# Performance work log

Measured on AMD Instinct MI355X. Metric: run time of the kernel, lower is better.

The kernel has to match this reference:

```python
import jax, jax.numpy as jnp
import numpy as np

# Model config (matches init_kwargs)
L_F, DELTA_F, L_S, DELTA_S = 1, 1, 32, 16
HIDDEN = 32       # SSM state dim H
GRU_H = 64        # slow-branch GRU hidden
N_GRU = 4
B, T = 4, 32768


def setup_inputs() -> dict:
    key = jax.random.key(0)
    ks = jax.random.split(key, 13)
    def nrm(k, shape, s=0.05):
        return jax.random.normal(k, shape, dtype=jnp.float32) * s
    return {
        "x": jax.random.normal(ks[0], (B, T), dtype=jnp.float32),
        # SlowBranch params
        "fc_in_w": nrm(ks[1], (GRU_H, 1), 0.3),
        "fc_in_b": nrm(ks[2], (GRU_H,)),
        "gru_wih": nrm(ks[3], (N_GRU, 3 * GRU_H, GRU_H), 0.1),
        "gru_whh": nrm(ks[4], (N_GRU, 3 * GRU_H, GRU_H), 0.1),
        "gru_bih": nrm(ks[5], (N_GRU, 3 * GRU_H)),
        "gru_bhh": nrm(ks[6], (N_GRU, 3 * GRU_H)),
        "out_fc_w": nrm(ks[7], (2 * HIDDEN, GRU_H), 0.1),
        "out_fc_b": nrm(ks[8], (2 * HIDDEN,)),
        # Fast branch params (F_IN: 1->H, F_OUT: H->1)
        "fin_w": nrm(ks[9], (HIDDEN, 1), 0.3),
        "fin_b": nrm(ks[10], (HIDDEN,)),
        "fout_w": nrm(ks[11], (1, HIDDEN), 0.1),
        "fout_b": nrm(ks[12], (1,)),
    }


def _gru_layer(xs, Wih, Whh, bih, bhh):
    """Torch-convention GRU layer. xs: (N, L, H_in) -> (N, L, H)."""
    H = Whh.shape[1]
    # Precompute input-side gate pre-activations: (N, L, 3H)
    xp = jnp.einsum('nlh,gh->nlg', xs, Wih) + bih
    def step(h, xt):
        gh = h @ Whh.T + bhh                       # (N, 3H)
        ir, iz, inew = jnp.split(xt, 3, axis=-1)
        hr, hz, hnew = jnp.split(gh, 3, axis=-1)
        r = jax.nn.sigmoid(ir + hr)
        z = jax.nn.sigmoid(iz + hz)
        n = jnp.tanh(inew + r * hnew)
        h = (1.0 - z) * n + z * h
        return h, h
    h0 = jnp.zeros((xs.shape[0], H), xs.dtype)
    _, ys = jax.lax.scan(step, h0, jnp.swapaxes(xp, 0, 1))  # (L, N, H)
    return jnp.swapaxes(ys, 0, 1)


def reference(x, fc_in_w, fc_in_b, gru_wih, gru_whh, gru_bih, gru_bhh,
              out_fc_w, out_fc_b, fin_w, fin_b, fout_w, fout_b):
    Bsz, Tlen = x.shape
    num_slow = (Tlen - L_S) // DELTA_S + 1

    frame_idx = jnp.arange(num_slow)[:, None] * DELTA_S + jnp.arange(L_S)[None, :]
    x_s = x[:, frame_idx].reshape(Bsz * num_slow, L_S, 1)      # (N, L_s, 1)
    h = jax.nn.relu(x_s * fc_in_w[:, 0] + fc_in_b)             # (N, L_s, GRU_H)
    for l in range(gru_wih.shape[0]):
        h = _gru_layer(h, gru_wih[l], gru_whh[l], gru_bih[l], gru_bhh[l])
    eps = h[:, -1, :] @ out_fc_w.T + out_fc_b                  # (N, 2H)
    eps = eps.reshape(Bsz, num_slow, 2 * HIDDEN)
    A_slow = jax.nn.sigmoid(eps[..., :HIDDEN])                 # (B, S, H)
    g_slow = eps[..., HIDDEN:]                                 # (B, S, H)

    # ---- Fast branch: per-sample diagonal linear SSM scan ----
    delta = DELTA_S // DELTA_F
    idx = jnp.clip(jnp.arange(Tlen) // delta - 1, 0, num_slow - 1)  # (T,)
    A_t = A_slow[:, idx, :]                                    # (B, T, H)
    u_t = (x[..., None] * fin_w[:, 0] + fin_b) * g_slow[:, idx, :]  # (B, T, H)

    def step(hc, inp):
        A, u = inp
        hn = A * hc + u
        return hn, hn
    h0 = jnp.zeros((Bsz, HIDDEN), x.dtype)
    _, h_all = jax.lax.scan(step, h0,
                            (jnp.swapaxes(A_t, 0, 1), jnp.swapaxes(u_t, 0, 1)))
    # h_all: (T, B, H); F_OUT applied to every state
    return jnp.einsum('tbh,h->bt', h_all, fout_w[0]) + fout_b[0]   # (B, T)
```

## Files before the change

kernel.cpp:

```cpp
#include <hip/hip_runtime.h>
#include <hip/hip_bf16.h>

typedef __bf16 bf16x8 __attribute__((ext_vector_type(8)));
typedef short short8 __attribute__((ext_vector_type(8)));
typedef float f32x4 __attribute__((ext_vector_type(4)));
typedef unsigned short ushort_t;

#define T_LEN 32768
#define B_SZ 4
#define NSLOW 2047
#define NSEQ (B_SZ * NSLOW)
#define GH 64
#define G3 192
#define NL 4
#define HID 32
#define NCH 256
#define L2E 1.44269504088896341f

#define OFF_X    0
#define OFF_FCW  131072
#define OFF_FCB  131136
#define OFF_WIH  131200
#define OFF_WHH  180352
#define OFF_BIH  229504
#define OFF_BHH  230272
#define OFF_OFW  231040
#define OFF_OFB  235136
#define OFF_FINW 235200
#define OFF_FINB 235232
#define OFF_FOW  235264
#define OFF_FOB  235296
#define CONV_TOTAL 235297
#define CONV_PAD_BYTES 470656

static __device__ __forceinline__ float bf2f(ushort_t u) {
    union { unsigned u; float f; } c; c.u = ((unsigned)u) << 16; return c.f;
}
static __device__ __forceinline__ ushort_t f2bf(float f) {
    union { float f; unsigned u; } c; c.f = f;
    unsigned r = (c.u + 0x7FFFu + ((c.u >> 16) & 1u)) >> 16;
    return (ushort_t)r;
}
static __device__ __forceinline__ unsigned pk2bf(float a, float b) {
    float2 f; f.x = a; f.y = b;
    __hip_bfloat162 h = __float22bfloat162_rn(f);
    unsigned u;
    __builtin_memcpy(&u, &h, 4);
    return u;
}
static __device__ __forceinline__ f32x4 mfma16(short8 a, short8 b, f32x4 c) {
    return __builtin_amdgcn_mfma_f32_16x16x32_bf16(
        __builtin_bit_cast(bf16x8, a), __builtin_bit_cast(bf16x8, b), c, 0, 0, 0);
}
static __device__ __forceinline__ int xoff(int t, int kb, int seq) {
    return ((((t << 3) + kb) << 4) + (seq ^ (kb & 7))) << 3;
}
static __device__ __forceinline__ short8 load_frag_scaled(const ushort_t* p, float s) {
    uint4 r = *(const uint4*)p;
    unsigned aa[4] = {r.x, r.y, r.z, r.w};
    short8 o;
#pragma unroll
    for (int i = 0; i < 4; ++i) {
        o[2 * i]     = (short)f2bf(bf2f((ushort_t)(aa[i] & 0xffffu)) * s);
        o[2 * i + 1] = (short)f2bf(bf2f((ushort_t)(aa[i] >> 16)) * s);
    }
    return o;
}

struct Ptrs13 { const void* p[13]; };

__global__ __launch_bounds__(256) void convert_kernel(Ptrs13 ptrs,
                                                      int* __restrict__ flag,
                                                      ushort_t* __restrict__ dst)
{
    __shared__ int scnt;
    if (threadIdx.x == 0) scnt = 0;
    __syncthreads();
    {
        ushort_t u = ((const ushort_t*)ptrs.p[0])[threadIdx.x];
        int e = (u >> 7) & 0xFF;
        int ok = (e >= 80 && e <= 141) ? 1 : 0;
#pragma unroll
        for (int d = 1; d < 64; d <<= 1) ok += __shfl_xor(ok, d, 64);
        if ((threadIdx.x & 63) == 0) atomicAdd(&scnt, ok);
    }
    __syncthreads();
    const bool isbf = (scnt >= 224);
    if (blockIdx.x == 0 && threadIdx.x == 0) *flag = isbf ? 1 : 0;

    const int offs[14] = {OFF_X, OFF_FCW, OFF_FCB, OFF_WIH, OFF_WHH, OFF_BIH,
                          OFF_BHH, OFF_OFW, OFF_OFB, OFF_FINW, OFF_FINB,
                          OFF_FOW, OFF_FOB, CONV_TOTAL};
    for (int idx = blockIdx.x * 256 + threadIdx.x; idx < CONV_TOTAL;
         idx += gridDim.x * 256) {
        int s = 0;
#pragma unroll
        for (int j = 1; j < 13; ++j) if (idx >= offs[j]) s = j;
        int k = idx - offs[s];
        ushort_t v = isbf ? ((const ushort_t*)ptrs.p[s])[k]
                          : f2bf(((const float*)ptrs.p[s])[k]);
        dst[idx] = v;
    }
}

__global__ __launch_bounds__(256, 2) void gru_kernel(
    const ushort_t* __restrict__ x, const ushort_t* __restrict__ fcw,
    const ushort_t* __restrict__ fcb, const ushort_t* __restrict__ wih,
    const ushort_t* __restrict__ whh, const ushort_t* __restrict__ bih,
    const ushort_t* __restrict__ bhh, const ushort_t* __restrict__ ofw,
    const ushort_t* __restrict__ ofb, float* __restrict__ Aslow,
    float* __restrict__ gslow)
{
    __shared__ short8 Xs8[4096];
    short* Xs = (short*)Xs8;
    const int tid = threadIdx.x;
    const int w = tid >> 6, lane = tid & 63;
    const int q = lane >> 4, m = lane & 15;
    const int jb = w * 16;
    const int n0 = blockIdx.x * 16;

#pragma unroll 1
    for (int ii = 0; ii < 16; ++ii) {
        int cid = ii * 256 + tid;
        int seq = cid & 15, kb = (cid >> 4) & 7, t = cid >> 7;
        int n = n0 + seq; if (n > NSEQ - 1) n = NSEQ - 1;
        int b = n / NSLOW, s = n - b * NSLOW;
        float xv = bf2f(x[b * T_LEN + s * 16 + t]);
        short8 v;
#pragma unroll
        for (int i = 0; i < 8; ++i) {
            int g = kb * 8 + i;
            float h = fmaf(xv, bf2f(fcw[g]), bf2f(fcb[g]));
            h = h > 0.f ? h : 0.f;
            v[i] = (short)f2bf(h);
        }
        Xs8[xoff(t, kb, seq) >> 3] = v;
    }

    const int col0 = jb + 4 * q;
    const int kbw = (col0 >> 3);
    const int wsub = (col0 & 7);
    const int kofs = q * 8;
    const int wbase0 = ((kbw << 4) + (m ^ (kbw & 7))) * 8 + wsub;

    float hc[4];
#pragma unroll 1
    for (int l = 0; l < NL; ++l) {
        const ushort_t* wl = wih + l * G3 * GH;
        const ushort_t* ul = whh + l * G3 * GH;
        short8 wR0 = load_frag_scaled(wl + (0 * 64 + jb + m) * 64 + kofs, -L2E);
        short8 wR1 = load_frag_scaled(wl + (0 * 64 + jb + m) * 64 + 32 + kofs, -L2E);
        short8 wZ0 = load_frag_scaled(wl + (1 * 64 + jb + m) * 64 + kofs, -L2E);
        short8 wZ1 = load_frag_scaled(wl + (1 * 64 + jb + m) * 64 + 32 + kofs, -L2E);
        short8 wN0 = load_frag_scaled(wl + (2 * 64 + jb + m) * 64 + kofs, 2.f * L2E);
        short8 wN1 = load_frag_scaled(wl + (2 * 64 + jb + m) * 64 + 32 + kofs, 2.f * L2E);
        short8 uR0 = load_frag_scaled(ul + (0 * 64 + jb + m) * 64 + kofs, -L2E);
        short8 uR1 = load_frag_scaled(ul + (0 * 64 + jb + m) * 64 + 32 + kofs, -L2E);
        short8 uZ0 = load_frag_scaled(ul + (1 * 64 + jb + m) * 64 + kofs, -L2E);
        short8 uZ1 = load_frag_scaled(ul + (1 * 64 + jb + m) * 64 + 32 + kofs, -L2E);
        short8 uN0 = load_frag_scaled(ul + (2 * 64 + jb + m) * 64 + kofs, 2.f * L2E);
        short8 uN1 = load_frag_scaled(ul + (2 * 64 + jb + m) * 64 + 32 + kofs, 2.f * L2E);

        f32x4 bRv, bZv, bNXv, bNHv;
#pragma unroll
        for (int i = 0; i < 4; ++i) {
            int c = col0 + i;
            bRv[i]  = -L2E * (bf2f(bih[l * G3 + c]) + bf2f(bhh[l * G3 + c]));
            bZv[i]  = -L2E * (bf2f(bih[l * G3 + 64 + c]) + bf2f(bhh[l * G3 + 64 + c]));
            bNXv[i] = 2.f * L2E * bf2f(bih[l * G3 + 128 + c]);
            bNHv[i] = 2.f * L2E * bf2f(bhh[l * G3 + 128 + c]);
        }

        hc[0] = hc[1] = hc[2] = hc[3] = 0.f;

        __syncthreads();
        int iA = xoff(0, q, m) >> 3;
        int iB = xoff(0, 4 + q, m) >> 3;
        int wb = wbase0;

        short8 cx0 = Xs8[iA], cx1 = Xs8[iB];
        short8 nx0 = Xs8[iA + 128], nx1 = Xs8[iB + 128];
        f32x4 xR = bRv, xZ = bZv, xN = bNXv;
        xR = mfma16(wR0, cx0, xR); xR = mfma16(wR1, cx1, xR);
        xZ = mfma16(wZ0, cx0, xZ); xZ = mfma16(wZ1, cx1, xZ);
        xN = mfma16(wN0, cx0, xN); xN = mfma16(wN1, cx1, xN);
#pragma unroll
        for (int i = 0; i < 4; ++i) {
            float r = __builtin_amdgcn_rcpf(1.f + __builtin_amdgcn_exp2f(xR[i]));
            float z = __builtin_amdgcn_rcpf(1.f + __builtin_amdgcn_exp2f(xZ[i]));
            float yp = fmaf(r, bNHv[i], xN[i]);
            float nn = fmaf(-2.f,
                __builtin_amdgcn_rcpf(1.f + __builtin_amdgcn_exp2f(yp)), 1.f);
            hc[i] = fmaf(z, hc[i] - nn, nn);
        }
        *(uint2*)(Xs + wb) = make_uint2(pk2bf(hc[0], hc[1]), pk2bf(hc[2], hc[3]));
        xR = bRv; xZ = bZv; xN = bNXv;
        xR = mfma16(wR0, nx0, xR); xR = mfma16(wR1, nx1, xR);
        xZ = mfma16(wZ0, nx0, xZ); xZ = mfma16(wZ1, nx1, xZ);
        xN = mfma16(wN0, nx0, xN); xN = mfma16(wN1, nx1, xN);
        iA += 128; iB += 128; wb += 1024;

#pragma unroll 1
        for (int t = 1; t < 32; ++t) {
            __syncthreads();
            short8 bh0 = Xs8[iA - 128];
            short8 bh1 = Xs8[iB - 128];
            short8 px0, px1;
            if (t < 31) {
                px0 = Xs8[iA + 128];
                px1 = Xs8[iB + 128];
            }
            f32x4 aR = xR, aZ = xZ, aNH = bNHv;
            aR  = mfma16(uR0, bh0, aR);  aR  = mfma16(uR1, bh1, aR);
            aZ  = mfma16(uZ0, bh0, aZ);  aZ  = mfma16(uZ1, bh1, aZ);
            aNH = mfma16(uN0, bh0, aNH); aNH = mfma16(uN1, bh1, aNH);
#pragma unroll
            for (int i = 0; i < 4; ++i) {
                float r = __builtin_amdgcn_rcpf(1.f + __builtin_amdgcn_exp2f(aR[i]));
                float z = __builtin_amdgcn_rcpf(1.f + __builtin_amdgcn_exp2f(aZ[i]));
                float yp = fmaf(r, aNH[i], xN[i]);
                float nn = fmaf(-2.f,
                    __builtin_amdgcn_rcpf(1.f + __builtin_amdgcn_exp2f(yp)), 1.f);
                hc[i] = fmaf(z, hc[i] - nn, nn);
            }
            *(uint2*)(Xs + wb) =
                make_uint2(pk2bf(hc[0], hc[1]), pk2bf(hc[2], hc[3]));
            if (t < 31) {
                xR = bRv; xZ = bZv; xN = bNXv;
                xR = mfma16(wR0, px0, xR); xR = mfma16(wR1, px1, xR);
                xZ = mfma16(wZ0, px0, xZ); xZ = mfma16(wZ1, px1, xZ);
                xN = mfma16(wN0, px0, xN); xN = mfma16(wN1, px1, xN);
            }
            iA += 128; iB += 128; wb += 1024;
        }
    }

    __syncthreads();
    short8 aL0 = Xs8[xoff(31, q, m) >> 3];
    short8 aL1 = Xs8[xoff(31, 4 + q, m) >> 3];
    float sc = (w < 2) ? -L2E : 1.f;
    short8 o0 = load_frag_scaled(ofw + (jb + m) * 64 + kofs, sc);
    short8 o1 = load_frag_scaled(ofw + (jb + m) * 64 + 32 + kofs, sc);
    f32x4 aE = {bf2f(ofb[col0]) * sc, bf2f(ofb[col0 + 1]) * sc,
                bf2f(ofb[col0 + 2]) * sc, bf2f(ofb[col0 + 3]) * sc};
    aE = mfma16(o0, aL0, aE);
    aE = mfma16(o1, aL1, aE);
    int n = n0 + m;
    if (w < 2) {
        f32x4 v;
#pragma unroll
        for (int i = 0; i < 4; ++i)
            v[i] = __builtin_amdgcn_rcpf(1.f + __builtin_amdgcn_exp2f(aE[i]));
        *(f32x4*)(Aslow + n * HID + col0) = v;
    } else {
        *(f32x4*)(gslow + n * HID + (col0 - 32)) = aE;
    }
}

__global__ __launch_bounds__(256) void pass1_kernel(
    const ushort_t* __restrict__ x, const float* __restrict__ Aslow,
    const float* __restrict__ gslow, const ushort_t* __restrict__ finw,
    const ushort_t* __restrict__ finb, float* __restrict__ P,
    float* __restrict__ S)
{
    int gt = blockIdx.x * 256 + threadIdx.x;
    int h = gt & 31, c = (gt >> 5) & 255, b = gt >> 13;
    float fw = bf2f(finw[h]), fb = bf2f(finb[h]);
    float Pv = 1.f, Sv = 0.f;
    int t0 = c * 128;
#pragma unroll 1
    for (int seg = 0; seg < 8; ++seg) {
        int sidx = (t0 >> 4) + seg - 1;
        if (sidx < 0) sidx = 0;
        if (sidx > NSLOW - 1) sidx = NSLOW - 1;
        float A = Aslow[(b * NSLOW + sidx) * HID + h];
        float g = gslow[(b * NSLOW + sidx) * HID + h];
        float fwg = fw * g, fbg = fb * g;
        const uint4* px = (const uint4*)(x + b * T_LEN + t0 + seg * 16);
        uint4 ra = px[0], rb = px[1];
        unsigned xa[8] = {ra.x, ra.y, ra.z, ra.w, rb.x, rb.y, rb.z, rb.w};
#pragma unroll
        for (int j = 0; j < 8; ++j) {
            float x0 = bf2f((ushort_t)(xa[j] & 0xffffu));
            float x1 = bf2f((ushort_t)(xa[j] >> 16));
            Sv = fmaf(A, Sv, fmaf(x0, fwg, fbg));
            Sv = fmaf(A, Sv, fmaf(x1, fwg, fbg));
        }
        float A2 = A * A, A4 = A2 * A2, A8 = A4 * A4;
        Pv *= A8 * A8;
    }
    P[(b * HID + h) * NCH + c] = Pv;
    S[(b * HID + h) * NCH + c] = Sv;
}

__global__ __launch_bounds__(128) void scan_kernel(
    const float* __restrict__ P, const float* __restrict__ S,
    float* __restrict__ Hpre)
{
    int tid = threadIdx.x;
    const float4* p4 = (const float4*)(P + tid * NCH);
    const float4* s4 = (const float4*)(S + tid * NCH);
    float* hp = Hpre + tid * NCH;
    float hr = 0.f;
#pragma unroll 8
    for (int c = 0; c < NCH / 4; ++c) {
        float4 pv = p4[c], sv = s4[c];
        hp[4 * c + 0] = hr; hr = fmaf(pv.x, hr, sv.x);
        hp[4 * c + 1] = hr; hr = fmaf(pv.y, hr, sv.y);
        hp[4 * c + 2] = hr; hr = fmaf(pv.z, hr, sv.z);
        hp[4 * c + 3] = hr; hr = fmaf(pv.w, hr, sv.w);
    }
}

__global__ __launch_bounds__(256) void pass2_kernel(
    const ushort_t* __restrict__ x, const float* __restrict__ Aslow,
    const float* __restrict__ gslow, const float* __restrict__ Hpre,
    const ushort_t* __restrict__ finw, const ushort_t* __restrict__ finb,
    const ushort_t* __restrict__ fow, const ushort_t* __restrict__ fob,
    const int* __restrict__ flag, void* __restrict__ outv)
{
    int wv = blockIdx.x * 4 + (threadIdx.x >> 6);
    int lane = threadIdx.x & 63;
    int half = lane >> 5, h = lane & 31;
    int pair = wv * 2 + half;
    int b = pair >> 8, c = pair & 255;
    const bool isbf = (*flag != 0);
    ushort_t* outb = (ushort_t*)outv;
    float* outf = (float*)outv;
    float hv = Hpre[(b * HID + h) * NCH + c];
    float fw = bf2f(finw[h]), fb = bf2f(finb[h]);
    float wo = bf2f(fow[h]), ob = bf2f(fob[0]);
    int t0 = c * 128;
#pragma unroll 1
    for (int blk = 0; blk < 4; ++blk) {
        float ykeep = 0.f;
        float A = 0.f, fwg = 0.f, fbg = 0.f;
#pragma unroll
        for (int tt = 0; tt < 32; ++tt) {
            int t = t0 + blk * 32 + tt;
            if ((tt & 15) == 0) {
                int sidx = (t >> 4) - 1;
                if (sidx < 0) sidx = 0;
                A = Aslow[(b * NSLOW + sidx) * HID + h];
                float g = gslow[(b * NSLOW + sidx) * HID + h];
                fwg = fw * g; fbg = fb * g;
            }
            float xv = bf2f(x[b * T_LEN + t]);
            hv = fmaf(A, hv, fmaf(xv, fwg, fbg));
            float y = hv * wo;
            y += __shfl_xor(y, 1, 64);
            y += __shfl_xor(y, 2, 64);
            y += __shfl_xor(y, 4, 64);
            y += __shfl_xor(y, 8, 64);
            y += __shfl_xor(y, 16, 64);
            if (tt == h) ykeep = y + ob;
        }
        int oidx = b * T_LEN + t0 + blk * 32 + h;
        if (isbf) outb[oidx] = f2bf(ykeep);
        else      outf[oidx] = ykeep;
    }
}

extern "C" void kernel_launch(void* const* d_in, const int* in_sizes, int n_in,
                              void* d_out, int out_size, void* d_ws, size_t ws_size,
                              hipStream_t stream)
{
    ushort_t* cv = (ushort_t*)d_ws;
    const ushort_t* x    = cv + OFF_X;
    const ushort_t* fcw  = cv + OFF_FCW;
    const ushort_t* fcb  = cv + OFF_FCB;
    const ushort_t* wih  = cv + OFF_WIH;
    const ushort_t* whh  = cv + OFF_WHH;
    const ushort_t* bih  = cv + OFF_BIH;
    const ushort_t* bhh  = cv + OFF_BHH;
    const ushort_t* ofw  = cv + OFF_OFW;
    const ushort_t* ofb  = cv + OFF_OFB;
    const ushort_t* finw = cv + OFF_FINW;
    const ushort_t* finb = cv + OFF_FINB;
    const ushort_t* fow  = cv + OFF_FOW;
    const ushort_t* fob  = cv + OFF_FOB;

    float* Aslow = (float*)((char*)d_ws + CONV_PAD_BYTES);
    float* gslow = Aslow + 8192 * 32;
    float* P     = gslow + 8192 * 32;
    float* S     = P + 4 * 32 * NCH;
    float* Hpre  = S + 4 * 32 * NCH;
    int*   flag  = (int*)(Hpre + 4 * 32 * NCH);

    Ptrs13 ptrs;
    for (int i = 0; i < 13; ++i) ptrs.p[i] = d_in[i];

    convert_kernel<<<dim3(920), dim3(256), 0, stream>>>(ptrs, flag, cv);
    gru_kernel<<<dim3(512), dim3(256), 0, stream>>>(
        x, fcw, fcb, wih, whh, bih, bhh, ofw, ofb, Aslow, gslow);
    pass1_kernel<<<dim3(128), dim3(256), 0, stream>>>(
        x, Aslow, gslow, finw, finb, P, S);
    scan_kernel<<<dim3(1), dim3(128), 0, stream>>>(P, S, Hpre);
    pass2_kernel<<<dim3(128), dim3(256), 0, stream>>>(
        x, Aslow, gslow, Hpre, finw, finb, fow, fob, flag, d_out);
}
```

Measured before the change: 193.1 us.

## Drop convert and scan kernels; read raw inputs and fold chunk scan into pass2

Removes the separate conversion kernel by having each kernel read the original inputs directly, with dtype detection moved into the GRU kernel and templated bf16/fp32 paths. Also removes the single-block scan kernel: each pass2 thread now serially combines the preceding chunk summaries itself, and P/S are stored in a chunk-major layout so those reads are coalesced. This cuts two launches and a full-input copy, at the cost of redundant prefix work in pass2 and wider fp32 loads of the raw inputs. Precision also changes slightly because x is no longer rounded to bf16 when the inputs are fp32.

```diff
diff --git a/kernel.cpp b/kernel.cpp
--- a/kernel.cpp
+++ b/kernel.cpp
@@ -16,21 +16,6 @@
 #define HID 32
 #define NCH 256
 #define L2E 1.44269504088896341f
-
-#define OFF_X    0
-#define OFF_FCW  131072
-#define OFF_FCB  131136
-#define OFF_WIH  131200
-#define OFF_WHH  180352
-#define OFF_BIH  229504
-#define OFF_BHH  230272
-#define OFF_OFW  231040
-#define OFF_OFB  235136
-#define OFF_FINW 235200
-#define OFF_FINB 235232
-#define OFF_FOW  235264
-#define OFF_FOB  235296
-#define CONV_TOTAL 235297
 #define CONV_PAD_BYTES 470656
 
 static __device__ __forceinline__ float bf2f(ushort_t u) {
@@ -55,87 +40,94 @@
 static __device__ __forceinline__ int xoff(int t, int kb, int seq) {
     return ((((t << 3) + kb) << 4) + (seq ^ (kb & 7))) << 3;
 }
-static __device__ __forceinline__ short8 load_frag_scaled(const ushort_t* p, float s) {
-    uint4 r = *(const uint4*)p;
-    unsigned aa[4] = {r.x, r.y, r.z, r.w};
+
+static __device__ __forceinline__ float ld1(const void* p, int i, bool isbf) {
+    return isbf ? bf2f(((const ushort_t*)p)[i]) : ((const float*)p)[i];
+}
+template<bool ISBF>
+static __device__ __forceinline__ float ld1t(const void* p, int i) {
+    if constexpr (ISBF) return bf2f(((const ushort_t*)p)[i]);
+    else return ((const float*)p)[i];
+}
+static __device__ __forceinline__ short8 load_frag_any(const void* p, int off,
+                                                       float s, bool isbf) {
     short8 o;
-#pragma unroll
-    for (int i = 0; i < 4; ++i) {
-        o[2 * i]     = (short)f2bf(bf2f((ushort_t)(aa[i] & 0xffffu)) * s);
-        o[2 * i + 1] = (short)f2bf(bf2f((ushort_t)(aa[i] >> 16)) * s);
+    if (isbf) {
+        uint4 r = *(const uint4*)((const ushort_t*)p + off);
+        unsigned aa[4] = {r.x, r.y, r.z, r.w};
+#pragma unroll
+        for (int i = 0; i < 4; ++i) {
+            o[2 * i]     = (short)f2bf(bf2f((ushort_t)(aa[i] & 0xffffu)) * s);
+            o[2 * i + 1] = (short)f2bf(bf2f((ushort_t)(aa[i] >> 16)) * s);
+        }
+    } else {
+        const float* f = (const float*)p + off;
+        float4 a = *(const float4*)f, b = *(const float4*)(f + 4);
+        o[0] = (short)f2bf(a.x * s); o[1] = (short)f2bf(a.y * s);
+        o[2] = (short)f2bf(a.z * s); o[3] = (short)f2bf(a.w * s);
+        o[4] = (short)f2bf(b.x * s); o[5] = (short)f2bf(b.y * s);
+        o[6] = (short)f2bf(b.z * s); o[7] = (short)f2bf(b.w * s);
     }
     return o;
 }
 
-struct Ptrs13 { const void* p[13]; };
-
-__global__ __launch_bounds__(256) void convert_kernel(Ptrs13 ptrs,
-                                                      int* __restrict__ flag,
-                                                      ushort_t* __restrict__ dst)
-{
-    __shared__ int scnt;
-    if (threadIdx.x == 0) scnt = 0;
-    __syncthreads();
-    {
-        ushort_t u = ((const ushort_t*)ptrs.p[0])[threadIdx.x];
-        int e = (u >> 7) & 0xFF;
-        int ok = (e >= 80 && e <= 141) ? 1 : 0;
-#pragma unroll
-        for (int d = 1; d < 64; d <<= 1) ok += __shfl_xor(ok, d, 64);
-        if ((threadIdx.x & 63) == 0) atomicAdd(&scnt, ok);
-    }
-    __syncthreads();
-    const bool isbf = (scnt >= 224);
-    if (blockIdx.x == 0 && threadIdx.x == 0) *flag = isbf ? 1 : 0;
-
-    const int offs[14] = {OFF_X, OFF_FCW, OFF_FCB, OFF_WIH, OFF_WHH, OFF_BIH,
-                          OFF_BHH, OFF_OFW, OFF_OFB, OFF_FINW, OFF_FINB,
-                          OFF_FOW, OFF_FOB, CONV_TOTAL};
-    for (int idx = blockIdx.x * 256 + threadIdx.x; idx < CONV_TOTAL;
-         idx += gridDim.x * 256) {
-        int s = 0;
-#pragma unroll
-        for (int j = 1; j < 13; ++j) if (idx >= offs[j]) s = j;
-        int k = idx - offs[s];
-        ushort_t v = isbf ? ((const ushort_t*)ptrs.p[s])[k]
-                          : f2bf(((const float*)ptrs.p[s])[k]);
-        dst[idx] = v;
-    }
-}
-
-__global__ __launch_bounds__(256, 2) void gru_kernel(
-    const ushort_t* __restrict__ x, const ushort_t* __restrict__ fcw,
-    const ushort_t* __restrict__ fcb, const ushort_t* __restrict__ wih,
-    const ushort_t* __restrict__ whh, const ushort_t* __restrict__ bih,
-    const ushort_t* __restrict__ bhh, const ushort_t* __restrict__ ofw,
-    const ushort_t* __restrict__ ofb, float* __restrict__ Aslow,
-    float* __restrict__ gslow)
-{
-    __shared__ short8 Xs8[4096];
-    short* Xs = (short*)Xs8;
-    const int tid = threadIdx.x;
-    const int w = tid >> 6, lane = tid & 63;
-    const int q = lane >> 4, m = lane & 15;
-    const int jb = w * 16;
-    const int n0 = blockIdx.x * 16;
-
+template<bool ISBF>
+static __device__ __forceinline__ void gru_fill(short8* Xs8, const void* x,
+        const void* fcw, const void* fcb, int n0, int tid)
+{
 #pragma unroll 1
     for (int ii = 0; ii < 16; ++ii) {
         int cid = ii * 256 + tid;
         int seq = cid & 15, kb = (cid >> 4) & 7, t = cid >> 7;
         int n = n0 + seq; if (n > NSEQ - 1) n = NSEQ - 1;
         int b = n / NSLOW, s = n - b * NSLOW;
-        float xv = bf2f(x[b * T_LEN + s * 16 + t]);
+        float xv = ld1t<ISBF>(x, b * T_LEN + s * 16 + t);
         short8 v;
 #pragma unroll
         for (int i = 0; i < 8; ++i) {
             int g = kb * 8 + i;
-            float h = fmaf(xv, bf2f(fcw[g]), bf2f(fcb[g]));
+            float h = fmaf(xv, ld1t<ISBF>(fcw, g), ld1t<ISBF>(fcb, g));
             h = h > 0.f ? h : 0.f;
             v[i] = (short)f2bf(h);
         }
         Xs8[xoff(t, kb, seq) >> 3] = v;
     }
+}
+
+__global__ __launch_bounds__(256, 2) void gru_kernel(
+    const void* __restrict__ x, const void* __restrict__ fcw,
+    const void* __restrict__ fcb, const void* __restrict__ wih,
+    const void* __restrict__ whh, const void* __restrict__ bih,
+    const void* __restrict__ bhh, const void* __restrict__ ofw,
+    const void* __restrict__ ofb, int* __restrict__ flag,
+    float* __restrict__ Aslow, float* __restrict__ gslow)
+{
+    __shared__ short8 Xs8[4096];
+    __shared__ int scnt;
+    short* Xs = (short*)Xs8;
+    const int tid = threadIdx.x;
+
+    if (tid == 0) scnt = 0;
+    __syncthreads();
+    {
+        ushort_t u = ((const ushort_t*)x)[tid];
+        int e = (u >> 7) & 0xFF;
+        int ok = (e >= 80 && e <= 141) ? 1 : 0;
+#pragma unroll
+        for (int d = 1; d < 64; d <<= 1) ok += __shfl_xor(ok, d, 64);
+        if ((tid & 63) == 0) atomicAdd(&scnt, ok);
+    }
+    __syncthreads();
+    const bool isbf = (scnt >= 224);
+    if (blockIdx.x == 0 && tid == 0) *flag = isbf ? 1 : 0;
+
+    const int w = tid >> 6, lane = tid & 63;
+    const int q = lane >> 4, m = lane & 15;
+    const int jb = w * 16;
+    const int n0 = blockIdx.x * 16;
+
+    if (isbf) gru_fill<true>(Xs8, x, fcw, fcb, n0, tid);
+    else      gru_fill<false>(Xs8, x, fcw, fcb, n0, tid);
 
     const int col0 = jb + 4 * q;
     const int kbw = (col0 >> 3);
@@ -146,29 +138,28 @@
     float hc[4];
 #pragma unroll 1
     for (int l = 0; l < NL; ++l) {
-        const ushort_t* wl = wih + l * G3 * GH;
-        const ushort_t* ul = whh + l * G3 * GH;
-        short8 wR0 = load_frag_scaled(wl + (0 * 64 + jb + m) * 64 + kofs, -L2E);
-        short8 wR1 = load_frag_scaled(wl + (0 * 64 + jb + m) * 64 + 32 + kofs, -L2E);
-        short8 wZ0 = load_frag_scaled(wl + (1 * 64 + jb + m) * 64 + kofs, -L2E);
-        short8 wZ1 = load_frag_scaled(wl + (1 * 64 + jb + m) * 64 + 32 + kofs, -L2E);
-        short8 wN0 = load_frag_scaled(wl + (2 * 64 + jb + m) * 64 + kofs, 2.f * L2E);
-        short8 wN1 = load_frag_scaled(wl + (2 * 64 + jb + m) * 64 + 32 + kofs, 2.f * L2E);
-        short8 uR0 = load_frag_scaled(ul + (0 * 64 + jb + m) * 64 + kofs, -L2E);
-        short8 uR1 = load_frag_scaled(ul + (0 * 64 + jb + m) * 64 + 32 + kofs, -L2E);
-        short8 uZ0 = load_frag_scaled(ul + (1 * 64 + jb + m) * 64 + kofs, -L2E);
-        short8 uZ1 = load_frag_scaled(ul + (1 * 64 + jb + m) * 64 + 32 + kofs, -L2E);
-        short8 uN0 = load_frag_scaled(ul + (2 * 64 + jb + m) * 64 + kofs, 2.f * L2E);
-        short8 uN1 = load_frag_scaled(ul + (2 * 64 + jb + m) * 64 + 32 + kofs, 2.f * L2E);
+        const int wb0 = l * G3 * GH;
+        short8 wR0 = load_frag_any(wih, wb0 + (0 * 64 + jb + m) * 64 + kofs, -L2E, isbf);
+        short8 wR1 = load_frag_any(wih, wb0 + (0 * 64 + jb + m) * 64 + 32 + kofs, -L2E, isbf);
+        short8 wZ0 = load_frag_any(wih, wb0 + (1 * 64 + jb + m) * 64 + kofs, -L2E, isbf);
+        short8 wZ1 = load_frag_any(wih, wb0 + (1 * 64 + jb + m) * 64 + 32 + kofs, -L2E, isbf);
+        short8 wN0 = load_frag_any(wih, wb0 + (2 * 64 + jb + m) * 64 + kofs, 2.f * L2E, isbf);
+        short8 wN1 = load_frag_any(wih, wb0 + (2 * 64 + jb + m) * 64 + 32 + kofs, 2.f * L2E, isbf);
+        short8 uR0 = load_frag_any(whh, wb0 + (0 * 64 + jb + m) * 64 + kofs, -L2E, isbf);
+        short8 uR1 = load_frag_any(whh, wb0 + (0 * 64 + jb + m) * 64 + 32 + kofs, -L2E, isbf);
+        short8 uZ0 = load_frag_any(whh, wb0 + (1 * 64 + jb + m) * 64 + kofs, -L2E, isbf);
+        short8 uZ1 = load_frag_any(whh, wb0 + (1 * 64 + jb + m) * 64 + 32 + kofs, -L2E, isbf);
+        short8 uN0 = load_frag_any(whh, wb0 + (2 * 64 + jb + m) * 64 + kofs, 2.f * L2E, isbf);
+        short8 uN1 = load_frag_any(whh, wb0 + (2 * 64 + jb + m) * 64 + 32 + kofs, 2.f * L2E, isbf);
 
         f32x4 bRv, bZv, bNXv, bNHv;
 #pragma unroll
         for (int i = 0; i < 4; ++i) {
             int c = col0 + i;
-            bRv[i]  = -L2E * (bf2f(bih[l * G3 + c]) + bf2f(bhh[l * G3 + c]));
-            bZv[i]  = -L2E * (bf2f(bih[l * G3 + 64 + c]) + bf2f(bhh[l * G3 + 64 + c]));
-            bNXv[i] = 2.f * L2E * bf2f(bih[l * G3 + 128 + c]);
-            bNHv[i] = 2.f * L2E * bf2f(bhh[l * G3 + 128 + c]);
+            bRv[i]  = -L2E * (ld1(bih, l * G3 + c, isbf) + ld1(bhh, l * G3 + c, isbf));
+            bZv[i]  = -L2E * (ld1(bih, l * G3 + 64 + c, isbf) + ld1(bhh, l * G3 + 64 + c, isbf));
+            bNXv[i] = 2.f * L2E * ld1(bih, l * G3 + 128 + c, isbf);
+            bNHv[i] = 2.f * L2E * ld1(bhh, l * G3 + 128 + c, isbf);
         }
 
         hc[0] = hc[1] = hc[2] = hc[3] = 0.f;
@@ -239,10 +230,10 @@
     short8 aL0 = Xs8[xoff(31, q, m) >> 3];
     short8 aL1 = Xs8[xoff(31, 4 + q, m) >> 3];
     float sc = (w < 2) ? -L2E : 1.f;
-    short8 o0 = load_frag_scaled(ofw + (jb + m) * 64 + kofs, sc);
-    short8 o1 = load_frag_scaled(ofw + (jb + m) * 64 + 32 + kofs, sc);
-    f32x4 aE = {bf2f(ofb[col0]) * sc, bf2f(ofb[col0 + 1]) * sc,
-                bf2f(ofb[col0 + 2]) * sc, bf2f(ofb[col0 + 3]) * sc};
+    short8 o0 = load_frag_any(ofw, (jb + m) * 64 + kofs, sc, isbf);
+    short8 o1 = load_frag_any(ofw, (jb + m) * 64 + 32 + kofs, sc, isbf);
+    f32x4 aE = {ld1(ofb, col0, isbf) * sc, ld1(ofb, col0 + 1, isbf) * sc,
+                ld1(ofb, col0 + 2, isbf) * sc, ld1(ofb, col0 + 3, isbf) * sc};
     aE = mfma16(o0, aL0, aE);
     aE = mfma16(o1, aL1, aE);
     int n = n0 + m;
@@ -257,15 +248,14 @@
     }
 }
 
-__global__ __launch_bounds__(256) void pass1_kernel(
-    const ushort_t* __restrict__ x, const float* __restrict__ Aslow,
-    const float* __restrict__ gslow, const ushort_t* __restrict__ finw,
-    const ushort_t* __restrict__ finb, float* __restrict__ P,
-    float* __restrict__ S)
+template<bool ISBF>
+static __device__ __forceinline__ void pass1_body(
+    const void* x, const float* Aslow, const float* gslow,
+    const void* finw, const void* finb, float* P, float* S)
 {
     int gt = blockIdx.x * 256 + threadIdx.x;
     int h = gt & 31, c = (gt >> 5) & 255, b = gt >> 13;
-    float fw = bf2f(finw[h]), fb = bf2f(finb[h]);
+    float fw = ld1t<ISBF>(finw, h), fb = ld1t<ISBF>(finb, h);
     float Pv = 1.f, Sv = 0.f;
     int t0 = c * 128;
 #pragma unroll 1
@@ -276,60 +266,68 @@
         float A = Aslow[(b * NSLOW + sidx) * HID + h];
         float g = gslow[(b * NSLOW + sidx) * HID + h];
         float fwg = fw * g, fbg = fb * g;
-        const uint4* px = (const uint4*)(x + b * T_LEN + t0 + seg * 16);
-        uint4 ra = px[0], rb = px[1];
-        unsigned xa[8] = {ra.x, ra.y, ra.z, ra.w, rb.x, rb.y, rb.z, rb.w};
-#pragma unroll
-        for (int j = 0; j < 8; ++j) {
-            float x0 = bf2f((ushort_t)(xa[j] & 0xffffu));
-            float x1 = bf2f((ushort_t)(xa[j] >> 16));
-            Sv = fmaf(A, Sv, fmaf(x0, fwg, fbg));
-            Sv = fmaf(A, Sv, fmaf(x1, fwg, fbg));
-        }
+        float xs[16];
+        if constexpr (ISBF) {
+            const uint4* px = (const uint4*)((const ushort_t*)x + b * T_LEN + t0 + seg * 16);
+            uint4 ra = px[0], rb = px[1];
+            unsigned xa[8] = {ra.x, ra.y, ra.z, ra.w, rb.x, rb.y, rb.z, rb.w};
+#pragma unroll
+            for (int j = 0; j < 8; ++j) {
+                xs[2 * j]     = bf2f((ushort_t)(xa[j] & 0xffffu));
+                xs[2 * j + 1] = bf2f((ushort_t)(xa[j] >> 16));
+            }
+        } else {
+            const float4* px = (const float4*)((const float*)x + b * T_LEN + t0 + seg * 16);
+#pragma unroll
+            for (int k = 0; k < 4; ++k) {
+                float4 v = px[k];
+                xs[4 * k] = v.x; xs[4 * k + 1] = v.y;
+                xs[4 * k + 2] = v.z; xs[4 * k + 3] = v.w;
+            }
+        }
+#pragma unroll
+        for (int j = 0; j < 16; ++j)
+            Sv = fmaf(A, Sv, fmaf(xs[j], fwg, fbg));
         float A2 = A * A, A4 = A2 * A2, A8 = A4 * A4;
         Pv *= A8 * A8;
     }
-    P[(b * HID + h) * NCH + c] = Pv;
-    S[(b * HID + h) * NCH + c] = Sv;
-}
-
-__global__ __launch_bounds__(128) void scan_kernel(
-    const float* __restrict__ P, const float* __restrict__ S,
-    float* __restrict__ Hpre)
-{
-    int tid = threadIdx.x;
-    const float4* p4 = (const float4*)(P + tid * NCH);
-    const float4* s4 = (const float4*)(S + tid * NCH);
-    float* hp = Hpre + tid * NCH;
-    float hr = 0.f;
-#pragma unroll 8
-    for (int c = 0; c < NCH / 4; ++c) {
-        float4 pv = p4[c], sv = s4[c];
-        hp[4 * c + 0] = hr; hr = fmaf(pv.x, hr, sv.x);
-        hp[4 * c + 1] = hr; hr = fmaf(pv.y, hr, sv.y);
-        hp[4 * c + 2] = hr; hr = fmaf(pv.z, hr, sv.z);
-        hp[4 * c + 3] = hr; hr = fmaf(pv.w, hr, sv.w);
-    }
-}
-
-__global__ __launch_bounds__(256) void pass2_kernel(
-    const ushort_t* __restrict__ x, const float* __restrict__ Aslow,
-    const float* __restrict__ gslow, const float* __restrict__ Hpre,
-    const ushort_t* __restrict__ finw, const ushort_t* __restrict__ finb,
-    const ushort_t* __restrict__ fow, const ushort_t* __restrict__ fob,
-    const int* __restrict__ flag, void* __restrict__ outv)
+    P[(b * NCH + c) * HID + h] = Pv;
+    S[(b * NCH + c) * HID + h] = Sv;
+}
+
+__global__ __launch_bounds__(256) void pass1_kernel(
+    const void* __restrict__ x, const float* __restrict__ Aslow,
+    const float* __restrict__ gslow, const void* __restrict__ finw,
+    const void* __restrict__ finb, const int* __restrict__ flag,
+    float* __restrict__ P, float* __restrict__ S)
+{
+    if (*flag) pass1_body<true>(x, Aslow, gslow, finw, finb, P, S);
+    else       pass1_body<false>(x, Aslow, gslow, finw, finb, P, S);
+}
+
+template<bool ISBF>
+static __device__ __forceinline__ void pass2_body(
+    const void* x, const float* Aslow, const float* gslow,
+    const float* P, const float* S, const void* finw, const void* finb,
+    const void* fow, const void* fob, void* outv)
 {
     int wv = blockIdx.x * 4 + (threadIdx.x >> 6);
     int lane = threadIdx.x & 63;
     int half = lane >> 5, h = lane & 31;
     int pair = wv * 2 + half;
     int b = pair >> 8, c = pair & 255;
-    const bool isbf = (*flag != 0);
     ushort_t* outb = (ushort_t*)outv;
     float* outf = (float*)outv;
-    float hv = Hpre[(b * HID + h) * NCH + c];
-    float fw = bf2f(finw[h]), fb = bf2f(finb[h]);
-    float wo = bf2f(fow[h]), ob = bf2f(fob[0]);
+    float fw = ld1t<ISBF>(finw, h), fb = ld1t<ISBF>(finb, h);
+    float wo = ld1t<ISBF>(fow, h), ob = ld1t<ISBF>(fob, 0);
+
+    float hv = 0.f;
+    const float* Pb = P + b * NCH * HID + h;
+    const float* Sb = S + b * NCH * HID + h;
+#pragma unroll 4
+    for (int j = 0; j < c; ++j)
+        hv = fmaf(Pb[j * HID], hv, Sb[j * HID]);
+
     int t0 = c * 128;
 #pragma unroll 1
     for (int blk = 0; blk < 4; ++blk) {
@@ -345,7 +343,7 @@
                 float g = gslow[(b * NSLOW + sidx) * HID + h];
                 fwg = fw * g; fbg = fb * g;
             }
-            float xv = bf2f(x[b * T_LEN + t]);
+            float xv = ld1t<ISBF>(x, b * T_LEN + t);
             hv = fmaf(A, hv, fmaf(xv, fwg, fbg));
             float y = hv * wo;
             y += __shfl_xor(y, 1, 64);
@@ -356,29 +354,40 @@
             if (tt == h) ykeep = y + ob;
         }
         int oidx = b * T_LEN + t0 + blk * 32 + h;
-        if (isbf) outb[oidx] = f2bf(ykeep);
-        else      outf[oidx] = ykeep;
-    }
+        if constexpr (ISBF) outb[oidx] = f2bf(ykeep);
+        else                outf[oidx] = ykeep;
+    }
+}
+
+__global__ __launch_bounds__(256) void pass2_kernel(
+    const void* __restrict__ x, const float* __restrict__ Aslow,
+    const float* __restrict__ gslow, const float* __restrict__ P,
+    const float* __restrict__ S, const void* __restrict__ finw,
+    const void* __restrict__ finb, const void* __restrict__ fow,
+    const void* __restrict__ fob, const int* __restrict__ flag,
+    void* __restrict__ outv)
+{
+    if (*flag) pass2_body<true>(x, Aslow, gslow, P, S, finw, finb, fow, fob, outv);
+    else       pass2_body<false>(x, Aslow, gslow, P, S, finw, finb, fow, fob, outv);
 }
 
 extern "C" void kernel_launch(void* const* d_in, const int* in_sizes, int n_in,
                               void* d_out, int out_size, void* d_ws, size_t ws_size,
                               hipStream_t stream)
 {
-    ushort_t* cv = (ushort_t*)d_ws;
-    const ushort_t* x    = cv + OFF_X;
-    const ushort_t* fcw  = cv + OFF_FCW;
-    const ushort_t* fcb  = cv + OFF_FCB;
-    const ushort_t* wih  = cv + OFF_WIH;
-    const ushort_t* whh  = cv + OFF_WHH;
-    const ushort_t* bih  = cv + OFF_BIH;
-    const ushort_t* bhh  = cv + OFF_BHH;
-    const ushort_t* ofw  = cv + OFF_OFW;
-    const ushort_t* ofb  = cv + OFF_OFB;
-    const ushort_t* finw = cv + OFF_FINW;
-    const ushort_t* finb = cv + OFF_FINB;
-    const ushort_t* fow  = cv + OFF_FOW;
-    const ushort_t* fob  = cv + OFF_FOB;
+    const void* x    = d_in[0];
+    const void* fcw  = d_in[1];
+    const void* fcb  = d_in[2];
+    const void* wih  = d_in[3];
+    const void* whh  = d_in[4];
+    const void* bih  = d_in[5];
+    const void* bhh  = d_in[6];
+    const void* ofw  = d_in[7];
+    const void* ofb  = d_in[8];
+    const void* finw = d_in[9];
+    const void* finb = d_in[10];
+    const void* fow  = d_in[11];
+    const void* fob  = d_in[12];
 
     float* Aslow = (float*)((char*)d_ws + CONV_PAD_BYTES);
     float* gslow = Aslow + 8192 * 32;
@@ -387,15 +396,10 @@
     float* Hpre  = S + 4 * 32 * NCH;
     int*   flag  = (int*)(Hpre + 4 * 32 * NCH);
 
-    Ptrs13 ptrs;
-    for (int i = 0; i < 13; ++i) ptrs.p[i] = d_in[i];
-
-    convert_kernel<<<dim3(920), dim3(256), 0, stream>>>(ptrs, flag, cv);
     gru_kernel<<<dim3(512), dim3(256), 0, stream>>>(
-        x, fcw, fcb, wih, whh, bih, bhh, ofw, ofb, Aslow, gslow);
+        x, fcw, fcb, wih, whh, bih, bhh, ofw, ofb, flag, Aslow, gslow);
     pass1_kernel<<<dim3(128), dim3(256), 0, stream>>>(
-        x, Aslow, gslow, finw, finb, P, S);
-    scan_kernel<<<dim3(1), dim3(128), 0, stream>>>(P, S, Hpre);
+        x, Aslow, gslow, finw, finb, flag, P, S);
     pass2_kernel<<<dim3(128), dim3(256), 0, stream>>>(
-        x, Aslow, gslow, Hpre, finw, finb, fow, fob, flag, d_out);
-}
+        x, Aslow, gslow, P, S, finw, finb, fow, fob, flag, d_out);
+}
```

New measurement: 210.1 us. 1.09x slower.

## Process two 16-sequence tiles per GRU block to interleave independent recurrences

Applied to the files above, without the earlier changes.

Each GRU block now handles 32 sequences as two independent 16-sequence tiles (A and B) with interleaved MFMA and gate math, doubling LDS to 128KB and halving the grid to 256 blocks. The aim is to hide the serial MFMA→transcendental→LDS latency chain of the recurrence with instruction-level parallelism and to amortise barriers and weight-fragment loads over twice the work. In exchange, occupancy drops to one block per CU, register pressure roughly doubles, and with 256 blocks on 256 CUs any tail or imbalance matters more.

```diff
diff --git a/kernel.cpp b/kernel.cpp
--- a/kernel.cpp
+++ b/kernel.cpp
@@ -103,7 +103,7 @@
     }
 }
 
-__global__ __launch_bounds__(256, 2) void gru_kernel(
+__global__ __launch_bounds__(256, 1) void gru_kernel(
     const ushort_t* __restrict__ x, const ushort_t* __restrict__ fcw,
     const ushort_t* __restrict__ fcb, const ushort_t* __restrict__ wih,
     const ushort_t* __restrict__ whh, const ushort_t* __restrict__ bih,
@@ -111,19 +111,21 @@
     const ushort_t* __restrict__ ofb, float* __restrict__ Aslow,
     float* __restrict__ gslow)
 {
-    __shared__ short8 Xs8[4096];
+    __shared__ short8 Xs8[8192];
     short* Xs = (short*)Xs8;
     const int tid = threadIdx.x;
     const int w = tid >> 6, lane = tid & 63;
     const int q = lane >> 4, m = lane & 15;
     const int jb = w * 16;
-    const int n0 = blockIdx.x * 16;
+    const int n0 = blockIdx.x * 32;
 
 #pragma unroll 1
-    for (int ii = 0; ii < 16; ++ii) {
+    for (int ii = 0; ii < 32; ++ii) {
         int cid = ii * 256 + tid;
-        int seq = cid & 15, kb = (cid >> 4) & 7, t = cid >> 7;
-        int n = n0 + seq; if (n > NSEQ - 1) n = NSEQ - 1;
+        int tl = cid >> 12, r = cid & 4095;
+        int seq = r & 15, kb = (r >> 4) & 7, t = r >> 7;
+        int n = n0 + tl * 16 + seq;
+        if (n > NSEQ - 1) n = NSEQ - 1;
         int b = n / NSLOW, s = n - b * NSLOW;
         float xv = bf2f(x[b * T_LEN + s * 16 + t]);
         short8 v;
@@ -134,7 +136,7 @@
             h = h > 0.f ? h : 0.f;
             v[i] = (short)f2bf(h);
         }
-        Xs8[xoff(t, kb, seq) >> 3] = v;
+        Xs8[(tl << 12) + (xoff(t, kb, seq) >> 3)] = v;
     }
 
     const int col0 = jb + 4 * q;
@@ -142,8 +144,10 @@
     const int wsub = (col0 & 7);
     const int kofs = q * 8;
     const int wbase0 = ((kbw << 4) + (m ^ (kbw & 7))) * 8 + wsub;
-
-    float hc[4];
+    const int iA0 = (q << 4) + (m ^ q);
+    const int iB0 = ((4 + q) << 4) + (m ^ ((4 + q) & 7));
+
+    float hcA[4], hcB[4];
 #pragma unroll 1
     for (int l = 0; l < NL; ++l) {
         const ushort_t* wl = wih + l * G3 * GH;
@@ -171,89 +175,130 @@
             bNHv[i] = 2.f * L2E * bf2f(bhh[l * G3 + 128 + c]);
         }
 
-        hc[0] = hc[1] = hc[2] = hc[3] = 0.f;
+#pragma unroll
+        for (int i = 0; i < 4; ++i) { hcA[i] = 0.f; hcB[i] = 0.f; }
 
         __syncthreads();
-        int iA = xoff(0, q, m) >> 3;
-        int iB = xoff(0, 4 + q, m) >> 3;
+        int iA = iA0, iB = iB0;
         int wb = wbase0;
 
-        short8 cx0 = Xs8[iA], cx1 = Xs8[iB];
-        short8 nx0 = Xs8[iA + 128], nx1 = Xs8[iB + 128];
-        f32x4 xR = bRv, xZ = bZv, xN = bNXv;
-        xR = mfma16(wR0, cx0, xR); xR = mfma16(wR1, cx1, xR);
-        xZ = mfma16(wZ0, cx0, xZ); xZ = mfma16(wZ1, cx1, xZ);
-        xN = mfma16(wN0, cx0, xN); xN = mfma16(wN1, cx1, xN);
+        short8 cxA0 = Xs8[iA],        cxA1 = Xs8[iB];
+        short8 cxB0 = Xs8[iA + 4096], cxB1 = Xs8[iB + 4096];
+        short8 nxA0 = Xs8[iA + 128],  nxA1 = Xs8[iB + 128];
+        short8 nxB0 = Xs8[iA + 4224], nxB1 = Xs8[iB + 4224];
+        f32x4 xRA = bRv, xZA = bZv, xNA = bNXv;
+        f32x4 xRB = bRv, xZB = bZv, xNB = bNXv;
+        xRA = mfma16(wR0, cxA0, xRA); xRA = mfma16(wR1, cxA1, xRA);
+        xRB = mfma16(wR0, cxB0, xRB); xRB = mfma16(wR1, cxB1, xRB);
+        xZA = mfma16(wZ0, cxA0, xZA); xZA = mfma16(wZ1, cxA1, xZA);
+        xZB = mfma16(wZ0, cxB0, xZB); xZB = mfma16(wZ1, cxB1, xZB);
+        xNA = mfma16(wN0, cxA0, xNA); xNA = mfma16(wN1, cxA1, xNA);
+        xNB = mfma16(wN0, cxB0, xNB); xNB = mfma16(wN1, cxB1, xNB);
 #pragma unroll
         for (int i = 0; i < 4; ++i) {
-            float r = __builtin_amdgcn_rcpf(1.f + __builtin_amdgcn_exp2f(xR[i]));
-            float z = __builtin_amdgcn_rcpf(1.f + __builtin_amdgcn_exp2f(xZ[i]));
-            float yp = fmaf(r, bNHv[i], xN[i]);
-            float nn = fmaf(-2.f,
-                __builtin_amdgcn_rcpf(1.f + __builtin_amdgcn_exp2f(yp)), 1.f);
-            hc[i] = fmaf(z, hc[i] - nn, nn);
-        }
-        *(uint2*)(Xs + wb) = make_uint2(pk2bf(hc[0], hc[1]), pk2bf(hc[2], hc[3]));
-        xR = bRv; xZ = bZv; xN = bNXv;
-        xR = mfma16(wR0, nx0, xR); xR = mfma16(wR1, nx1, xR);
-        xZ = mfma16(wZ0, nx0, xZ); xZ = mfma16(wZ1, nx1, xZ);
-        xN = mfma16(wN0, nx0, xN); xN = mfma16(wN1, nx1, xN);
+            float rA = __builtin_amdgcn_rcpf(1.f + __builtin_amdgcn_exp2f(xRA[i]));
+            float rB = __builtin_amdgcn_rcpf(1.f + __builtin_amdgcn_exp2f(xRB[i]));
+            float zA = __builtin_amdgcn_rcpf(1.f + __builtin_amdgcn_exp2f(xZA[i]));
+            float zB = __builtin_amdgcn_rcpf(1.f + __builtin_amdgcn_exp2f(xZB[i]));
+            float ypA = fmaf(rA, bNHv[i], xNA[i]);
+            float ypB = fmaf(rB, bNHv[i], xNB[i]);
+            float nnA = fmaf(-2.f,
+                __builtin_amdgcn_rcpf(1.f + __builtin_amdgcn_exp2f(ypA)), 1.f);
+            float nnB = fmaf(-2.f,
+                __builtin_amdgcn_rcpf(1.f + __builtin_amdgcn_exp2f(ypB)), 1.f);
+            hcA[i] = fmaf(zA, hcA[i] - nnA, nnA);
+            hcB[i] = fmaf(zB, hcB[i] - nnB, nnB);
+        }
+        *(uint2*)(Xs + wb) =
+            make_uint2(pk2bf(hcA[0], hcA[1]), pk2bf(hcA[2], hcA[3]));
+        *(uint2*)(Xs + wb + 32768) =
+            make_uint2(pk2bf(hcB[0], hcB[1]), pk2bf(hcB[2], hcB[3]));
+        xRA = bRv; xZA = bZv; xNA = bNXv;
+        xRB = bRv; xZB = bZv; xNB = bNXv;
+        xRA = mfma16(wR0, nxA0, xRA); xRA = mfma16(wR1, nxA1, xRA);
+        xRB = mfma16(wR0, nxB0, xRB); xRB = mfma16(wR1, nxB1, xRB);
+        xZA = mfma16(wZ0, nxA0, xZA); xZA = mfma16(wZ1, nxA1, xZA);
+        xZB = mfma16(wZ0, nxB0, xZB); xZB = mfma16(wZ1, nxB1, xZB);
+        xNA = mfma16(wN0, nxA0, xNA); xNA = mfma16(wN1, nxA1, xNA);
+        xNB = mfma16(wN0, nxB0, xNB); xNB = mfma16(wN1, nxB1, xNB);
         iA += 128; iB += 128; wb += 1024;
 
 #pragma unroll 1
         for (int t = 1; t < 32; ++t) {
             __syncthreads();
-            short8 bh0 = Xs8[iA - 128];
-            short8 bh1 = Xs8[iB - 128];
-            short8 px0, px1;
+            short8 bhA0 = Xs8[iA - 128],  bhA1 = Xs8[iB - 128];
+            short8 bhB0 = Xs8[iA + 3968], bhB1 = Xs8[iB + 3968];
+            short8 pxA0, pxA1, pxB0, pxB1;
             if (t < 31) {
-                px0 = Xs8[iA + 128];
-                px1 = Xs8[iB + 128];
+                pxA0 = Xs8[iA + 128];  pxA1 = Xs8[iB + 128];
+                pxB0 = Xs8[iA + 4224]; pxB1 = Xs8[iB + 4224];
             }
-            f32x4 aR = xR, aZ = xZ, aNH = bNHv;
-            aR  = mfma16(uR0, bh0, aR);  aR  = mfma16(uR1, bh1, aR);
-            aZ  = mfma16(uZ0, bh0, aZ);  aZ  = mfma16(uZ1, bh1, aZ);
-            aNH = mfma16(uN0, bh0, aNH); aNH = mfma16(uN1, bh1, aNH);
+            f32x4 aRA = xRA, aZA = xZA, aNHA = bNHv;
+            f32x4 aRB = xRB, aZB = xZB, aNHB = bNHv;
+            aRA  = mfma16(uR0, bhA0, aRA);  aRA  = mfma16(uR1, bhA1, aRA);
+            aRB  = mfma16(uR0, bhB0, aRB);  aRB  = mfma16(uR1, bhB1, aRB);
+            aZA  = mfma16(uZ0, bhA0, aZA);  aZA  = mfma16(uZ1, bhA1, aZA);
+            aZB  = mfma16(uZ0, bhB0, aZB);  aZB  = mfma16(uZ1, bhB1, aZB);
+            aNHA = mfma16(uN0, bhA0, aNHA); aNHA = mfma16(uN1, bhA1, aNHA);
+            aNHB = mfma16(uN0, bhB0, aNHB); aNHB = mfma16(uN1, bhB1, aNHB);
 #pragma unroll
             for (int i = 0; i < 4; ++i) {
-                float r = __builtin_amdgcn_rcpf(1.f + __builtin_amdgcn_exp2f(aR[i]));
-                float z = __builtin_amdgcn_rcpf(1.f + __builtin_amdgcn_exp2f(aZ[i]));
-                float yp = fmaf(r, aNH[i], xN[i]);
-                float nn = fmaf(-2.f,
-                    __builtin_amdgcn_rcpf(1.f + __builtin_amdgcn_exp2f(yp)), 1.f);
-                hc[i] = fmaf(z, hc[i] - nn, nn);
+                float rA = __builtin_amdgcn_rcpf(1.f + __builtin_amdgcn_exp2f(aRA[i]));
+                float rB = __builtin_amdgcn_rcpf(1.f + __builtin_amdgcn_exp2f(aRB[i]));
+                float zA = __builtin_amdgcn_rcpf(1.f + __builtin_amdgcn_exp2f(aZA[i]));
+                float zB = __builtin_amdgcn_rcpf(1.f + __builtin_amdgcn_exp2f(aZB[i]));
+                float ypA = fmaf(rA, aNHA[i], xNA[i]);
+                float ypB = fmaf(rB, aNHB[i], xNB[i]);
+                float nnA = fmaf(-2.f,
+                    __builtin_amdgcn_rcpf(1.f + __builtin_amdgcn_exp2f(ypA)), 1.f);
+                float nnB = fmaf(-2.f,
+                    __builtin_amdgcn_rcpf(1.f + __builtin_amdgcn_exp2f(ypB)), 1.f);
+                hcA[i] = fmaf(zA, hcA[i] - nnA, nnA);
+                hcB[i] = fmaf(zB, hcB[i] - nnB, nnB);
             }
             *(uint2*)(Xs + wb) =
-                make_uint2(pk2bf(hc[0], hc[1]), pk2bf(hc[2], hc[3]));
+                make_uint2(pk2bf(hcA[0], hcA[1]), pk2bf(hcA[2], hcA[3]));
+            *(uint2*)(Xs + wb + 32768) =
+                make_uint2(pk2bf(hcB[0], hcB[1]), pk2bf(hcB[2], hcB[3]));
             if (t < 31) {
-                xR = bRv; xZ = bZv; xN = bNXv;
-                xR = mfma16(wR0, px0, xR); xR = mfma16(wR1, px1, xR);
-                xZ = mfma16(wZ0, px0, xZ); xZ = mfma16(wZ1, px1, xZ);
-                xN = mfma16(wN0, px0, xN); xN = mfma16(wN1, px1, xN);
+                xRA = bRv; xZA = bZv; xNA = bNXv;
+                xRB = bRv; xZB = bZv; xNB = bNXv;
+                xRA = mfma16(wR0, pxA0, xRA); xRA = mfma16(wR1, pxA1, xRA);
+                xRB = mfma16(wR0, pxB0, xRB); xRB = mfma16(wR1, pxB1, xRB);
+                xZA = mfma16(wZ0, pxA0, xZA); xZA = mfma16(wZ1, pxA1, xZA);
+                xZB = mfma16(wZ0, pxB0, xZB); xZB = mfma16(wZ1, pxB1, xZB);
+                xNA = mfma16(wN0, pxA0, xNA); xNA = mfma16(wN1, pxA1, xNA);
+                xNB = mfma16(wN0, pxB0, xNB); xNB = mfma16(wN1, pxB1, xNB);
             }
             iA += 128; iB += 128; wb += 1024;
         }
     }
 
     __syncthreads();
-    short8 aL0 = Xs8[xoff(31, q, m) >> 3];
-    short8 aL1 = Xs8[xoff(31, 4 + q, m) >> 3];
+    short8 aLA0 = Xs8[(31 << 7) + iA0],        aLA1 = Xs8[(31 << 7) + iB0];
+    short8 aLB0 = Xs8[(31 << 7) + 4096 + iA0], aLB1 = Xs8[(31 << 7) + 4096 + iB0];
     float sc = (w < 2) ? -L2E : 1.f;
     short8 o0 = load_frag_scaled(ofw + (jb + m) * 64 + kofs, sc);
     short8 o1 = load_frag_scaled(ofw + (jb + m) * 64 + 32 + kofs, sc);
-    f32x4 aE = {bf2f(ofb[col0]) * sc, bf2f(ofb[col0 + 1]) * sc,
-                bf2f(ofb[col0 + 2]) * sc, bf2f(ofb[col0 + 3]) * sc};
-    aE = mfma16(o0, aL0, aE);
-    aE = mfma16(o1, aL1, aE);
-    int n = n0 + m;
+    f32x4 aEb = {bf2f(ofb[col0]) * sc, bf2f(ofb[col0 + 1]) * sc,
+                 bf2f(ofb[col0 + 2]) * sc, bf2f(ofb[col0 + 3]) * sc};
+    f32x4 aEA = aEb, aEB = aEb;
+    aEA = mfma16(o0, aLA0, aEA); aEA = mfma16(o1, aLA1, aEA);
+    aEB = mfma16(o0, aLB0, aEB); aEB = mfma16(o1, aLB1, aEB);
+    int nA = n0 + m;
+    int nB = n0 + 16 + m;
     if (w < 2) {
-        f32x4 v;
-#pragma unroll
-        for (int i = 0; i < 4; ++i)
-            v[i] = __builtin_amdgcn_rcpf(1.f + __builtin_amdgcn_exp2f(aE[i]));
-        *(f32x4*)(Aslow + n * HID + col0) = v;
+        f32x4 vA, vB;
+#pragma unroll
+        for (int i = 0; i < 4; ++i) {
+            vA[i] = __builtin_amdgcn_rcpf(1.f + __builtin_amdgcn_exp2f(aEA[i]));
+            vB[i] = __builtin_amdgcn_rcpf(1.f + __builtin_amdgcn_exp2f(aEB[i]));
+        }
+        *(f32x4*)(Aslow + nA * HID + col0) = vA;
+        *(f32x4*)(Aslow + nB * HID + col0) = vB;
     } else {
-        *(f32x4*)(gslow + n * HID + (col0 - 32)) = aE;
+        *(f32x4*)(gslow + nA * HID + (col0 - 32)) = aEA;
+        *(f32x4*)(gslow + nB * HID + (col0 - 32)) = aEB;
     }
 }
 
@@ -391,7 +436,7 @@
     for (int i = 0; i < 13; ++i) ptrs.p[i] = d_in[i];
 
     convert_kernel<<<dim3(920), dim3(256), 0, stream>>>(ptrs, flag, cv);
-    gru_kernel<<<dim3(512), dim3(256), 0, stream>>>(
+    gru_kernel<<<dim3(256), dim3(256), 0, stream>>>(
         x, fcw, fcb, wih, whh, bih, bhh, ofw, ofb, Aslow, gslow);
     pass1_kernel<<<dim3(128), dim3(256), 0, stream>>>(
         x, Aslow, gslow, finw, finb, P, S);
```

Result: slower. 215.1 us (+11.4%).
